# Kernel optimization log

Hardware: AMD Instinct MI355X
Metric: run time of the kernel (lower is better)

Reference implementation:

```python
import jax, jax.numpy as jnp
import numpy as np

TAU = 18.0


def smooth_compose(X, M, tau=TAU):
    # Z[n,i,j] = smooth_min(X[n,i], M[i,j]) = -(1/tau) * log(exp(-tau*X) + exp(-tau*M))
    # Y[n,j]   = (1/tau) * logsumexp(tau * Z[n,:,j], axis over i)
    # tau*Z = -logaddexp(-tau*X, -tau*M)  (numerically stable, same math)
    tZ = -jnp.logaddexp(-tau * X[:, :, None], -tau * M[None, :, :])  # [n, d, d]
    return (1.0 / tau) * jax.nn.logsumexp(tZ, axis=1)  # [n, d]


def setup_inputs() -> dict:
    key = jax.random.key(0)
    k1, k2, k3, k4, k5 = jax.random.split(key, 5)
    n, p, d = 2048, 1024, 256
    S = jax.random.uniform(k1, (n, p), dtype=jnp.float32)
    T = jax.random.uniform(k2, (n, p), dtype=jnp.float32)
    # learned parameters (A0/M0/B0 defaults are 0.5-filled; use random values of similar scale)
    A = jax.random.uniform(k3, (p, d), dtype=jnp.float32)
    # rawM = logit(M0); random small logits -> M = sigmoid(rawM) near 0.5
    rawM = 0.5 * jax.random.normal(k4, (d, d), dtype=jnp.float32)
    B = jax.random.uniform(k5, (d, p), dtype=jnp.float32)
    return {"S": S, "T": T, "A": A, "rawM": rawM, "B": B}


def reference(S, T, A, rawM, B):
    M = jax.nn.sigmoid(rawM)            # [d, d]
    X_hat = S @ A                       # [n, d]
    Y_hat = T @ A                       # [n, d]
    X_box = jnp.clip(X_hat, 0.0, 1.0)
    Y_box = jnp.clip(Y_hat, 0.0, 1.0)
    Y_pred = smooth_compose(X_box, M, tau=TAU)  # [n, d]
    S_rec = X_hat @ B                   # [n, p]
    T_rec = Y_hat @ B                   # [n, p]
    T_pred = Y_pred @ B                 # [n, p]
    return (X_hat, Y_hat, X_box, Y_box, Y_pred, S_rec, T_rec, T_pred)
```

## Files before the change

kernel.cpp:

```cpp
#include <hip/hip_runtime.h>
#include <math.h>

constexpr int N = 2048;
constexpr int P = 1024;
constexpr int D = 256;
constexpr float TAU = 18.0f;

constexpr size_t OFF_XHAT  = 0;
constexpr size_t OFF_YHAT  = (size_t)N * D;
constexpr size_t OFF_XBOX  = 2 * (size_t)N * D;
constexpr size_t OFF_YBOX  = 3 * (size_t)N * D;
constexpr size_t OFF_YPRED = 4 * (size_t)N * D;
constexpr size_t OFF_SREC  = 5 * (size_t)N * D;

constexpr size_t WS_ATH = 0;
constexpr size_t WS_ATL = 524288;
constexpr size_t WS_BTH = 1048576;
constexpr size_t WS_BTL = 1572864;
constexpr size_t WS_V   = 2097152;
constexpr size_t WS_U   = 2359296;
constexpr size_t WS_LHH = 4456448;
constexpr size_t WS_LHL = 7602176;
constexpr size_t WS_STH = 10747904;
constexpr size_t WS_STL = 19136512;

typedef short bhalf8 __attribute__((ext_vector_type(8)));
typedef float f32x4  __attribute__((ext_vector_type(4)));

__device__ inline short f2bf(float f) {
  union { float f; unsigned u; } x; x.f = f;
  unsigned r = (x.u + 0x7FFFu + ((x.u >> 16) & 1u)) >> 16;
  return (short)r;
}
__device__ inline float bf2f(short h) {
  union { unsigned u; float f; } x; x.u = ((unsigned)(unsigned short)h) << 16;
  return x.f;
}
__device__ inline int xcd_swz(int bid, int nwg) {
  const int cpx = nwg >> 3;
  return (bid & 7) * cpx + (bid >> 3);
}

__device__ inline void transpose_hilo_body(
    const float* __restrict__ src, short* __restrict__ dh,
    short* __restrict__ dl, int R, int C, int bx, int by, int t) {
  __shared__ __align__(16) float tile[32][36];
  const int r0 = bx * 32, c0 = by * 32;
  {
    const int tr = t >> 3, tc4 = (t & 7) * 4;
    float4 x = *(const float4*)(src + (size_t)(r0 + tr) * C + c0 + tc4);
    *(float4*)&tile[tr][tc4] = x;
  }
  __syncthreads();
  {
    const int tc = t >> 3, tr4 = (t & 7) * 4;
    short4 h, l;
    float f0 = tile[tr4 + 0][tc];
    float f1 = tile[tr4 + 1][tc];
    float f2 = tile[tr4 + 2][tc];
    float f3 = tile[tr4 + 3][tc];
    h.x = f2bf(f0); l.x = f2bf(f0 - bf2f(h.x));
    h.y = f2bf(f1); l.y = f2bf(f1 - bf2f(h.y));
    h.z = f2bf(f2); l.z = f2bf(f2 - bf2f(h.z));
    h.w = f2bf(f3); l.w = f2bf(f3 - bf2f(h.w));
    *(short4*)(dh + (size_t)(c0 + tc) * R + r0 + tr4) = h;
    *(short4*)(dl + (size_t)(c0 + tc) * R + r0 + tr4) = l;
  }
}

__global__ __launch_bounds__(256) void prep_all_kernel(
    const float* __restrict__ S, const float* __restrict__ Tm,
    const float* __restrict__ A, const float* __restrict__ rawM,
    const float* __restrict__ B, short* __restrict__ Ath,
    short* __restrict__ Atl, short* __restrict__ Bth,
    short* __restrict__ Btl, float* __restrict__ V,
    short* __restrict__ STh, short* __restrict__ STl) {
  const int bid = blockIdx.x;
  const int t = threadIdx.x;
  if (bid < 64) {
    const int idx = (bid * 256 + t) * 4;
    float4 x = *(const float4*)(rawM + idx);
    float4 o;
    o.x = expf(-TAU / (1.0f + expf(-x.x)));
    o.y = expf(-TAU / (1.0f + expf(-x.y)));
    o.z = expf(-TAU / (1.0f + expf(-x.z)));
    o.w = expf(-TAU / (1.0f + expf(-x.w)));
    *(float4*)(V + idx) = o;
  } else if (bid < 320) {
    const int idx = bid - 64;
    transpose_hilo_body(A, Ath, Atl, P, D, idx & 31, idx >> 5, t);
  } else if (bid < 576) {
    const int idx = bid - 320;
    transpose_hilo_body(B, Bth, Btl, D, P, idx & 7, idx >> 3, t);
  } else {
    const int idx = bid - 576;
#pragma unroll
    for (int q = 0; q < 4; ++q) {
      const int row = idx * 4 + q;
      const float* src = (row < N) ? (S + (size_t)row * P)
                                   : (Tm + (size_t)(row - N) * P);
      float4 x = *(const float4*)(src + t * 4);
      short4 h, l;
      h.x = f2bf(x.x); l.x = f2bf(x.x - bf2f(h.x));
      h.y = f2bf(x.y); l.y = f2bf(x.y - bf2f(h.y));
      h.z = f2bf(x.z); l.z = f2bf(x.z - bf2f(h.z));
      h.w = f2bf(x.w); l.w = f2bf(x.w - bf2f(h.w));
      *(short4*)(STh + (size_t)row * P + t * 4) = h;
      *(short4*)(STl + (size_t)row * P + t * 4) = l;
    }
  }
}

__global__ __launch_bounds__(256) void gemm1_mfma(
    const short* __restrict__ STh, const short* __restrict__ STl,
    const short* __restrict__ Ath, const short* __restrict__ Atl,
    float* __restrict__ out, float* __restrict__ U,
    short* __restrict__ LHh, short* __restrict__ LHl) {
  __shared__ __align__(16) short As_h[2][32][72];
  __shared__ __align__(16) short As_l[2][32][72];
  __shared__ __align__(16) short Bs_h[2][64][72];
  __shared__ __align__(16) short Bs_l[2][64][72];

  const int t  = threadIdx.x;
  const int wg = xcd_swz(blockIdx.x, 512);
  const int m0 = (wg >> 2) * 32, n0 = (wg & 3) * 64;

  const int arow = t >> 3;
  const int ak   = (t & 7) * 8;
  const short* AhR = STh + (size_t)(m0 + arow) * P;
  const short* AlR = STl + (size_t)(m0 + arow) * P;
  const int brow = t >> 2;
  const int bk   = (t & 3) * 16;
  const short* BhR = Ath + (size_t)(n0 + brow) * P;
  const short* BlR = Atl + (size_t)(n0 + brow) * P;

  const int l = t & 63, w = t >> 6;
  const int wr = (w & 1) * 16, wc = (w >> 1) * 32;
  const int fr = l & 15, ko8 = (l >> 4) * 8, rq = (l >> 4) * 4;

  f32x4 acc[2];
  acc[0] = (f32x4){0.f, 0.f, 0.f, 0.f};
  acc[1] = (f32x4){0.f, 0.f, 0.f, 0.f};

  bhalf8 pah, pal, pbh0, pbh1, pbl0, pbl1;
  pah  = *(const bhalf8*)(AhR + ak);
  pal  = *(const bhalf8*)(AlR + ak);
  pbh0 = *(const bhalf8*)(BhR + bk);
  pbh1 = *(const bhalf8*)(BhR + bk + 8);
  pbl0 = *(const bhalf8*)(BlR + bk);
  pbl1 = *(const bhalf8*)(BlR + bk + 8);

#define STAGE1(buf)                                   \
  do {                                                \
    *(bhalf8*)&As_h[buf][arow][ak]    = pah;          \
    *(bhalf8*)&As_l[buf][arow][ak]    = pal;          \
    *(bhalf8*)&Bs_h[buf][brow][bk]    = pbh0;         \
    *(bhalf8*)&Bs_h[buf][brow][bk+8]  = pbh1;         \
    *(bhalf8*)&Bs_l[buf][brow][bk]    = pbl0;         \
    *(bhalf8*)&Bs_l[buf][brow][bk+8]  = pbl1;         \
  } while (0)

  STAGE1(0);

  for (int ks = 0; ks < 16; ++ks) {
    const int b = ks & 1;
    if (ks < 15) {
      const int kn = (ks + 1) * 64;
      pah  = *(const bhalf8*)(AhR + kn + ak);
      pal  = *(const bhalf8*)(AlR + kn + ak);
      pbh0 = *(const bhalf8*)(BhR + kn + bk);
      pbh1 = *(const bhalf8*)(BhR + kn + bk + 8);
      pbl0 = *(const bhalf8*)(BlR + kn + bk);
      pbl1 = *(const bhalf8*)(BlR + kn + bk + 8);
    }
    __syncthreads();
#pragma unroll
    for (int ks2 = 0; ks2 < 2; ++ks2) {
      const int ko = ks2 * 32 + ko8;
      bhalf8 ahv = *(const bhalf8*)&As_h[b][wr + fr][ko];
      bhalf8 alv = *(const bhalf8*)&As_l[b][wr + fr][ko];
#pragma unroll
      for (int ni = 0; ni < 2; ++ni) {
        bhalf8 bhv = *(const bhalf8*)&Bs_h[b][wc + ni * 16 + fr][ko];
        bhalf8 blv = *(const bhalf8*)&Bs_l[b][wc + ni * 16 + fr][ko];
        acc[ni] = __builtin_amdgcn_mfma_f32_16x16x32_bf16(ahv, bhv, acc[ni], 0, 0, 0);
        acc[ni] = __builtin_amdgcn_mfma_f32_16x16x32_bf16(ahv, blv, acc[ni], 0, 0, 0);
        acc[ni] = __builtin_amdgcn_mfma_f32_16x16x32_bf16(alv, bhv, acc[ni], 0, 0, 0);
      }
    }
    if (ks < 15) STAGE1((ks + 1) & 1);
  }
#undef STAGE1

#pragma unroll
  for (int ni = 0; ni < 2; ++ni) {
    const int col = n0 + wc + ni * 16 + fr;
#pragma unroll
    for (int r = 0; r < 4; ++r) {
      const int row = m0 + wr + rq + r;
      const float v = acc[ni][r];
      const float c = fminf(fmaxf(v, 0.0f), 1.0f);
      const short h  = f2bf(v);
      const short lo = f2bf(v - bf2f(h));
      LHh[(size_t)row * D + col] = h;
      LHl[(size_t)row * D + col] = lo;
      if (row < N) {
        out[OFF_XHAT + (size_t)row * D + col] = v;
        out[OFF_XBOX + (size_t)row * D + col] = c;
        U[(size_t)row * D + col] = expf(-TAU * c);
      } else {
        const size_t ry = (size_t)(row - N);
        out[OFF_YHAT + ry * D + col] = v;
        out[OFF_YBOX + ry * D + col] = c;
      }
    }
  }
}

__global__ __launch_bounds__(256) void smooth_kernel(
    const float* __restrict__ U, const float* __restrict__ V,
    float* __restrict__ ypred, short* __restrict__ LHh,
    short* __restrict__ LHl) {
  __shared__ float us[256][34];
  const int t = threadIdx.x;
  const int n0 = blockIdx.x * 32, j0 = blockIdx.y * 32;

  {
    const int sr = t & 31;
    const int si = (t >> 5) * 32;
    const float* up = U + (size_t)(n0 + sr) * D + si;
#pragma unroll
    for (int q = 0; q < 32; q += 4) {
      float4 x = *(const float4*)(up + q);
      us[si + q + 0][sr] = x.x;
      us[si + q + 1][sr] = x.y;
      us[si + q + 2][sr] = x.z;
      us[si + q + 3][sr] = x.w;
    }
  }
  __syncthreads();

  const int jg = (t & 15) * 2;
  const int nn = (t >> 4) * 2;
  const float* vp = V + j0 + jg;

  float acc00 = 0.f, acc01 = 0.f, acc10 = 0.f, acc11 = 0.f;
#pragma unroll 8
  for (int i = 0; i < D; ++i) {
    float2 u2 = *(const float2*)&us[i][nn];
    float2 v2 = *(const float2*)(vp + (size_t)i * D);
    acc00 += __builtin_amdgcn_rcpf(u2.x + v2.x);
    acc01 += __builtin_amdgcn_rcpf(u2.x + v2.y);
    acc10 += __builtin_amdgcn_rcpf(u2.y + v2.x);
    acc11 += __builtin_amdgcn_rcpf(u2.y + v2.y);
  }

  float a[2][2] = {{acc00, acc01}, {acc10, acc11}};
#pragma unroll
  for (int pI = 0; pI < 2; ++pI) {
    const int row = n0 + nn + pI;
    float2 o;
    o.x = (1.0f / TAU) * logf(a[pI][0]);
    o.y = (1.0f / TAU) * logf(a[pI][1]);
    *(float2*)(ypred + (size_t)row * D + j0 + jg) = o;
    short2 h2, l2;
    h2.x = f2bf(o.x); l2.x = f2bf(o.x - bf2f(h2.x));
    h2.y = f2bf(o.y); l2.y = f2bf(o.y - bf2f(h2.y));
    const size_t lrow = (size_t)(2 * N + row) * D + j0 + jg;
    *(short2*)(LHh + lrow) = h2;
    *(short2*)(LHl + lrow) = l2;
  }
}

__global__ __launch_bounds__(512) void gemm2_mfma(
    const short* __restrict__ LHh, const short* __restrict__ LHl,
    const short* __restrict__ Bth, const short* __restrict__ Btl,
    float* __restrict__ rec) {
  __shared__ __align__(16) short As_h[2][128][40];
  __shared__ __align__(16) short As_l[2][128][40];
  __shared__ __align__(16) short Bs_h[2][64][40];
  __shared__ __align__(16) short Bs_l[2][64][40];

  const int t  = threadIdx.x;
  const int wg = xcd_swz(blockIdx.x, 768);
  const int m0 = (wg >> 4) * 128, n0 = (wg & 15) * 64;

  const int arow = t >> 2;
  const int ak   = (t & 3) * 8;
  const short* AhR = LHh + (size_t)(m0 + arow) * D;
  const short* AlR = LHl + (size_t)(m0 + arow) * D;
  const int brow = t >> 3;
  const int bk   = (t & 7) * 4;
  const short* BhR = Bth + (size_t)(n0 + brow) * D;
  const short* BlR = Btl + (size_t)(n0 + brow) * D;

  const int l = t & 63, w = t >> 6;
  const int wr = (w & 3) * 32, wc = (w >> 2) * 32;
  const int fr = l & 15, ko8 = (l >> 4) * 8, rq = (l >> 4) * 4;

  f32x4 acc[2][2];
#pragma unroll
  for (int i = 0; i < 2; ++i)
#pragma unroll
    for (int j = 0; j < 2; ++j) acc[i][j] = (f32x4){0.f, 0.f, 0.f, 0.f};

  bhalf8 pah, pal;
  short4 pbh, pbl;
  pah = *(const bhalf8*)(AhR + ak);
  pal = *(const bhalf8*)(AlR + ak);
  pbh = *(const short4*)(BhR + bk);
  pbl = *(const short4*)(BlR + bk);

#define STAGE2(buf)                            \
  do {                                         \
    *(bhalf8*)&As_h[buf][arow][ak] = pah;      \
    *(bhalf8*)&As_l[buf][arow][ak] = pal;      \
    *(short4*)&Bs_h[buf][brow][bk] = pbh;      \
    *(short4*)&Bs_l[buf][brow][bk] = pbl;      \
  } while (0)

  STAGE2(0);

  for (int ks = 0; ks < 8; ++ks) {
    const int b = ks & 1;
    if (ks < 7) {
      const int kn = (ks + 1) * 32;
      pah = *(const bhalf8*)(AhR + kn + ak);
      pal = *(const bhalf8*)(AlR + kn + ak);
      pbh = *(const short4*)(BhR + kn + bk);
      pbl = *(const short4*)(BlR + kn + bk);
    }
    __syncthreads();
    bhalf8 ahv[2], alv[2], bhv[2], blv[2];
#pragma unroll
    for (int mi = 0; mi < 2; ++mi) {
      ahv[mi] = *(const bhalf8*)&As_h[b][wr + mi * 16 + fr][ko8];
      alv[mi] = *(const bhalf8*)&As_l[b][wr + mi * 16 + fr][ko8];
      bhv[mi] = *(const bhalf8*)&Bs_h[b][wc + mi * 16 + fr][ko8];
      blv[mi] = *(const bhalf8*)&Bs_l[b][wc + mi * 16 + fr][ko8];
    }
#pragma unroll
    for (int mi = 0; mi < 2; ++mi)
#pragma unroll
      for (int ni = 0; ni < 2; ++ni) {
        acc[mi][ni] = __builtin_amdgcn_mfma_f32_16x16x32_bf16(ahv[mi], bhv[ni], acc[mi][ni], 0, 0, 0);
        acc[mi][ni] = __builtin_amdgcn_mfma_f32_16x16x32_bf16(ahv[mi], blv[ni], acc[mi][ni], 0, 0, 0);
        acc[mi][ni] = __builtin_amdgcn_mfma_f32_16x16x32_bf16(alv[mi], bhv[ni], acc[mi][ni], 0, 0, 0);
      }
    if (ks < 7) STAGE2((ks + 1) & 1);
  }
#undef STAGE2

#pragma unroll
  for (int mi = 0; mi < 2; ++mi)
#pragma unroll
    for (int ni = 0; ni < 2; ++ni) {
      const int col = n0 + wc + ni * 16 + fr;
#pragma unroll
      for (int r = 0; r < 4; ++r) {
        const int row = m0 + wr + mi * 16 + rq + r;
        rec[(size_t)row * P + col] = acc[mi][ni][r];
      }
    }
}

extern "C" void kernel_launch(void* const* d_in, const int* in_sizes, int n_in,
                              void* d_out, int out_size, void* d_ws,
                              size_t ws_size, hipStream_t stream) {
  const float* S    = (const float*)d_in[0];
  const float* T    = (const float*)d_in[1];
  const float* A    = (const float*)d_in[2];
  const float* rawM = (const float*)d_in[3];
  const float* B    = (const float*)d_in[4];
  float* out = (float*)d_out;
  char* ws = (char*)d_ws;

  short* Ath = (short*)(ws + WS_ATH);
  short* Atl = (short*)(ws + WS_ATL);
  short* Bth = (short*)(ws + WS_BTH);
  short* Btl = (short*)(ws + WS_BTL);
  float* V   = (float*)(ws + WS_V);
  float* U   = (float*)(ws + WS_U);
  short* LHh = (short*)(ws + WS_LHH);
  short* LHl = (short*)(ws + WS_LHL);
  short* STh = (short*)(ws + WS_STH);
  short* STl = (short*)(ws + WS_STL);

  prep_all_kernel<<<1600, 256, 0, stream>>>(S, T, A, rawM, B, Ath, Atl, Bth,
                                            Btl, V, STh, STl);
  gemm1_mfma<<<512, 256, 0, stream>>>(STh, STl, Ath, Atl, out, U, LHh, LHl);
  smooth_kernel<<<dim3(64, 8), 256, 0, stream>>>(U, V, out + OFF_YPRED, LHh,
                                                 LHl);
  gemm2_mfma<<<768, 512, 0, stream>>>(LHh, LHl, Bth, Btl, out + OFF_SREC);
}
```

Baseline: 133.7 us.

## Add runtime fast path for smooth_compose when all X_hat clip to one

gemm1 now also reduces the minimum of the X_hat values with wave shuffles and a global atomicMin, stored as an int in a new workspace slot. If that minimum is at least 1, every clipped X_box entry equals 1. The full smooth_kernel then exits early, and a new smooth_bcast kernel computes one Y_pred row from V and broadcasts it to all rows. Otherwise the original path runs, so results stay correct for any input. The cost is an extra kernel launch, a reduction plus atomic at the end of gemm1, and the full path is still paid when the condition fails.

Result: no change. 134.0 us (+0.3%).

```diff
diff --git a/kernel.cpp b/kernel.cpp
--- a/kernel.cpp
+++ b/kernel.cpp
@@ -23,6 +23,7 @@
 constexpr size_t WS_LHL = 7602176;
 constexpr size_t WS_STH = 10747904;
 constexpr size_t WS_STL = 19136512;
+constexpr size_t WS_MIN = 27525120;
 
 typedef short bhalf8 __attribute__((ext_vector_type(8)));
 typedef float f32x4  __attribute__((ext_vector_type(4)));
@@ -74,10 +75,12 @@
     const float* __restrict__ B, short* __restrict__ Ath,
     short* __restrict__ Atl, short* __restrict__ Bth,
     short* __restrict__ Btl, float* __restrict__ V,
-    short* __restrict__ STh, short* __restrict__ STl) {
+    short* __restrict__ STh, short* __restrict__ STl,
+    int* __restrict__ minx) {
   const int bid = blockIdx.x;
   const int t = threadIdx.x;
   if (bid < 64) {
+    if (bid == 0 && t == 0) *minx = 0x7F800000;
     const int idx = (bid * 256 + t) * 4;
     float4 x = *(const float4*)(rawM + idx);
     float4 o;
@@ -115,7 +118,8 @@
     const short* __restrict__ STh, const short* __restrict__ STl,
     const short* __restrict__ Ath, const short* __restrict__ Atl,
     float* __restrict__ out, float* __restrict__ U,
-    short* __restrict__ LHh, short* __restrict__ LHl) {
+    short* __restrict__ LHh, short* __restrict__ LHl,
+    int* __restrict__ minx) {
   __shared__ __align__(16) short As_h[2][32][72];
   __shared__ __align__(16) short As_l[2][32][72];
   __shared__ __align__(16) short Bs_h[2][64][72];
@@ -192,6 +196,7 @@
   }
 #undef STAGE1
 
+  float lmin = 3.0e38f;
 #pragma unroll
   for (int ni = 0; ni < 2; ++ni) {
     const int col = n0 + wc + ni * 16 + fr;
@@ -202,6 +207,7 @@
       const float c = fminf(fmaxf(v, 0.0f), 1.0f);
       const short h  = f2bf(v);
       const short lo = f2bf(v - bf2f(h));
+      lmin = fminf(lmin, v);
       LHh[(size_t)row * D + col] = h;
       LHl[(size_t)row * D + col] = lo;
       if (row < N) {
@@ -215,12 +221,18 @@
       }
     }
   }
+  if (m0 < N) {
+#pragma unroll
+    for (int off = 32; off; off >>= 1) lmin = fminf(lmin, __shfl_xor(lmin, off));
+    if (l == 0) atomicMin(minx, __float_as_int(lmin));
+  }
 }
 
 __global__ __launch_bounds__(256) void smooth_kernel(
     const float* __restrict__ U, const float* __restrict__ V,
     float* __restrict__ ypred, short* __restrict__ LHh,
-    short* __restrict__ LHl) {
+    short* __restrict__ LHl, const float* __restrict__ minx) {
+  if (*minx >= 1.0f) return;
   __shared__ float us[256][34];
   const int t = threadIdx.x;
   const int n0 = blockIdx.x * 32, j0 = blockIdx.y * 32;
@@ -272,6 +284,30 @@
   }
 }
 
+__global__ __launch_bounds__(256) void smooth_bcast(
+    const float* __restrict__ V, const float* __restrict__ minx,
+    float* __restrict__ ypred, short* __restrict__ LHh,
+    short* __restrict__ LHl) {
+  if (!(*minx >= 1.0f)) return;
+  const int t = threadIdx.x;
+  const float u0 = expf(-TAU);
+  float acc = 0.f;
+#pragma unroll 8
+  for (int i = 0; i < D; ++i)
+    acc += __builtin_amdgcn_rcpf(u0 + V[(size_t)i * D + t]);
+  const float y = (1.0f / TAU) * logf(acc);
+  const short h  = f2bf(y);
+  const short lo = f2bf(y - bf2f(h));
+  const int r0 = blockIdx.x * 8;
+#pragma unroll
+  for (int q = 0; q < 8; ++q) {
+    const int row = r0 + q;
+    ypred[(size_t)row * D + t] = y;
+    LHh[(size_t)(2 * N + row) * D + t] = h;
+    LHl[(size_t)(2 * N + row) * D + t] = lo;
+  }
+}
+
 __global__ __launch_bounds__(512) void gemm2_mfma(
     const short* __restrict__ LHh, const short* __restrict__ LHl,
     const short* __restrict__ Bth, const short* __restrict__ Btl,
@@ -385,11 +421,15 @@
   short* LHl = (short*)(ws + WS_LHL);
   short* STh = (short*)(ws + WS_STH);
   short* STl = (short*)(ws + WS_STL);
+  int*   mnx = (int*)(ws + WS_MIN);
 
   prep_all_kernel<<<1600, 256, 0, stream>>>(S, T, A, rawM, B, Ath, Atl, Bth,
-                                            Btl, V, STh, STl);
-  gemm1_mfma<<<512, 256, 0, stream>>>(STh, STl, Ath, Atl, out, U, LHh, LHl);
+                                            Btl, V, STh, STl, mnx);
+  gemm1_mfma<<<512, 256, 0, stream>>>(STh, STl, Ath, Atl, out, U, LHh, LHl,
+                                      mnx);
   smooth_kernel<<<dim3(64, 8), 256, 0, stream>>>(U, V, out + OFF_YPRED, LHh,
-                                                 LHl);
+                                                 LHl, (const float*)mnx);
+  smooth_bcast<<<256, 256, 0, stream>>>(V, (const float*)mnx, out + OFF_YPRED,
+                                        LHh, LHl);
   gemm2_mfma<<<768, 512, 0, stream>>>(LHh, LHl, Bth, Btl, out + OFF_SREC);
 }
```
